# Kernel tuning notes

Hardware: AMD Instinct MI355X
Metric: run time of the kernel (lower is better)

The kernel has to match this reference:

```python
import jax, jax.numpy as jnp
import numpy as np
from jax import lax

ROUTING_ITERS = 3
EPS = 1e-8


def _conv(x, w, b, stride=1):
    # x: [B,C,H,W], w: [O,C,kh,kw]  (VALID padding, NCHW/OIHW)
    y = lax.conv_general_dilated(x, w, (stride, stride), 'VALID',
                                 dimension_numbers=('NCHW', 'OIHW', 'NCHW'))
    return y + b[None, :, None, None]


def _maxpool2(x):
    return lax.reduce_window(x, -jnp.inf, lax.max, (1, 1, 2, 2), (1, 1, 2, 2), 'VALID')


def _squash(s, axis=-1):
    n2 = jnp.sum(s * s, axis=axis, keepdims=True)
    return s * (n2 / (1.0 + n2)) / jnp.sqrt(n2 + EPS)


def setup_inputs() -> dict:
    key = jax.random.key(0)
    ks = jax.random.split(key, 9)
    p = lambda k, shp: (jax.random.normal(k, shp, dtype=jnp.float32) * 0.05)
    return {
        'x':  jax.random.normal(ks[0], (64, 1, 92, 92), dtype=jnp.float32),
        'w1': p(ks[1], (128, 1, 9, 9)),   'b1': jnp.zeros((128,), jnp.float32),
        'w2': p(ks[2], (64, 128, 5, 5)),  'b2': jnp.zeros((64,), jnp.float32),
        'wc': p(ks[3], (128, 64, 8, 8)),  'bc': jnp.zeros((128,), jnp.float32),
        # routing transform: [num_primary=1024, num_sar=10, out_dim=16, in_dim=32]
        'Wr': p(ks[4], (1024, 10, 16, 32)),
    }


def reference(x, w1, b1, w2, b2, wc, bc, Wr):
    B = x.shape[0]
    # feature extractor (dropout is identity at inference)
    h = jax.nn.relu(_conv(x, w1, b1))          # [B,128,84,84]
    h = _maxpool2(h)                            # [B,128,42,42]
    h = _conv(h, w2, b2)                        # [B,64,38,38]
    # primary capsule conv
    h = _conv(h, wc, bc, stride=2)              # [B,128,16,16]
    # 128 channels = 4 capsule types * 32-dim capsules, 16x16 spatial -> 1024 caps
    u = h.reshape(B, 4, 32, 16, 16).transpose(0, 1, 3, 4, 2).reshape(B, 1024, 32)
    u = _squash(u)                              # [B,1024,32]
    # u_hat: predictions of each primary cap for each SAR cap
    u_hat = jnp.einsum('bpi,ptoi->bpto', u, Wr)  # [B,1024,10,16]
    # dynamic routing
    b_log = jnp.zeros((B, 1024, 10), dtype=x.dtype)
    for _ in range(ROUTING_ITERS):
        c = jax.nn.softmax(b_log, axis=2)               # [B,1024,10]
        s = jnp.einsum('bpt,bpto->bto', c, u_hat)       # [B,10,16]
        v = _squash(s)                                   # [B,10,16]
        b_log = b_log + jnp.einsum('bpto,bto->bpt', u_hat, v)
    likelihood = jnp.sqrt(jnp.sum(v * v, axis=-1) + EPS)  # [B,10]
    return likelihood
```

## Files before the change

### kernel.cpp

```cpp
#include <hip/hip_runtime.h>
#include <hip/hip_bf16.h>
#include <math.h>


#define EPSF 1e-8f

typedef __bf16 bf16x8 __attribute__((ext_vector_type(8)));
typedef __bf16 bf16x4 __attribute__((ext_vector_type(4)));
typedef float floatx4 __attribute__((ext_vector_type(4)));
typedef float floatx16 __attribute__((ext_vector_type(16)));

__global__ __launch_bounds__(256) void k_t_all(const float* __restrict__ Wr,
                                               const float* __restrict__ wc,
                                               const float* __restrict__ w2,
                                               const float* __restrict__ w1,
                                               __bf16* __restrict__ wrb,
                                               __bf16* __restrict__ wca,
                                               __bf16* __restrict__ w2a,
                                               __bf16* __restrict__ w1b) {
    int i = blockIdx.x * 256 + threadIdx.x;
    if (i < 5242880) {
        wrb[i] = (__bf16)Wr[i];
        return;
    }
    int i2 = i - 5242880;
    if (i2 < 524288) {
        int j = i2 & 7, lane = (i2 >> 3) & 63, f = i2 >> 9;
        int ct = f & 3, ks = (f >> 2) & 1, khw = (f >> 3) & 63, icc = f >> 9;
        int c32 = lane & 31, h = lane >> 5;
        int oc = ct * 32 + c32;
        int ic = icc * 32 + ks * 16 + h * 8 + j;
        wca[i2] = (__bf16)wc[(oc * 64 + ic) * 64 + khw];
        return;
    }
    int i3 = i2 - 524288;
    if (i3 < 204800) {
        int j = i3 & 7, lane = (i3 >> 3) & 63, f = i3 >> 9;
        int mt = f & 1, ks = (f >> 1) & 3, rem = f >> 3;
        int khw = rem % 25, icc = rem / 25;
        int c32 = lane & 31, h = lane >> 5;
        int oc = mt * 32 + c32;
        int ic = icc * 64 + ks * 16 + h * 8 + j;
        w2a[i3] = (__bf16)w2[(oc * 128 + ic) * 25 + khw];
        return;
    }
    int i4 = i3 - 204800;
    if (i4 < 12288) {
        int kt = i4 >> 10, oc = (i4 >> 3) & 127, j = i4 & 7;
        int k = kt * 8 + j;
        w1b[i4] = (__bf16)(k < 81 ? w1[oc * 81 + k] : 0.f);
    }
}

__global__ __launch_bounds__(256, 3) void k_conv1_mfma(const float* __restrict__ x,
                                                       const __bf16* __restrict__ w1b,
                                                       const float* __restrict__ b1,
                                                       __bf16* __restrict__ h1n) {
    __shared__ float xs[960];
    __shared__ __bf16 Bl[18432];
    int py = blockIdx.x, ocg = blockIdx.y, b = blockIdx.z;
    int t = threadIdx.x;
    int lane = t & 63, w = t >> 6;
    int cc = lane & 15, q = lane >> 4;

    const float* xb = x + (size_t)b * 8464 + 2 * py * 92;
    for (int j = t; j < 920; j += 256) xs[j] = xb[j];

    int ocA = ocg * 64 + w * 16 + cc;
    bf16x8 af[3];
#pragma unroll
    for (int ks = 0; ks < 3; ++ks)
        af[ks] = *(const bf16x8*)(w1b + ((ks * 4 + q) * 128 + ocA) * 8);

    __syncthreads();

    if (t < 192) {
        int row = t / 96, pos = t - (t / 96) * 96;
        int sbase = row * 92 + pos;
        bool pvalid = pos < 84;
#pragma unroll
        for (int kt = 0; kt < 12; ++kt) {
            bf16x8 pk;
#pragma unroll
            for (int j = 0; j < 8; ++j) {
                int k = kt * 8 + j;
                int kh = k / 9, kw = k - kh * 9;
                float v = (pvalid && k < 81) ? xs[sbase + kh * 92 + kw] : 0.f;
                pk[j] = (__bf16)v;
            }
            *(bf16x8*)(Bl + ((kt * 2 + row) * 96 + pos) * 8) = pk;
        }
    }
    __syncthreads();

    floatx4 acc[2][6];
    const char* Bb = (const char*)Bl + cc * 16 + q * 3072;
#pragma unroll
    for (int rr = 0; rr < 2; ++rr)
#pragma unroll
        for (int n6 = 0; n6 < 6; ++n6) {
            floatx4 a = (floatx4){0.f, 0.f, 0.f, 0.f};
#pragma unroll
            for (int ks = 0; ks < 3; ++ks) {
                bf16x8 bf = *(const bf16x8*)(Bb + ks * 12288 + rr * 1536 + n6 * 256);
                a = __builtin_amdgcn_mfma_f32_16x16x32_bf16(af[ks], bf, a, 0, 0, 0);
            }
            acc[rr][n6] = a;
        }

    int oc0 = ocg * 64 + w * 16 + q * 4;
    float4 bv = *(const float4*)(b1 + oc0);
    size_t obase = (((size_t)b * 42 + py) * 42) * 128 + oc0;
#pragma unroll
    for (int n6 = 0; n6 < 6; ++n6) {
        bf16x4 pk;
#pragma unroll
        for (int r = 0; r < 4; ++r) {
            float vert = fmaxf(acc[0][n6][r], acc[1][n6][r]);
            float hz = fmaxf(vert, __shfl_xor(vert, 1, 64));
            float pooled = fmaxf(hz + ((const float*)&bv)[r], 0.f);
            pk[r] = (__bf16)pooled;
        }
        if ((cc & 1) == 0) {
            int px = n6 * 8 + (cc >> 1);
            if (px < 42)
                *(bf16x4*)(h1n + obase + (size_t)px * 128) = pk;
        }
    }
}

__global__ __launch_bounds__(256) void k_conv2(const __bf16* __restrict__ h1n,
                                               const __bf16* __restrict__ w2a,
                                               float* __restrict__ p01) {
    __shared__ __bf16 ins[25704];
    int g = blockIdx.x, b = blockIdx.y, icc = blockIdx.z;
    int row0 = g * 5;
    int t = threadIdx.x;
    int lane = t & 63, w = t >> 6;
    int c32 = lane & 31, h = lane >> 5;
    int validp = (g < 7) ? 190 : 114;
    int ic0 = icc * 64;

    int baseN[2], posi[2];
#pragma unroll
    for (int nt = 0; nt < 2; ++nt) {
        int pi = (w * 2 + nt) * 32 + c32;
        int pc = pi < validp ? pi : validp - 1;
        int r = pc / 38, c = pc - r * 38;
        posi[nt] = pi;
        baseN[nt] = (r * 42 + c) * 136 + h * 16;
    }

#pragma unroll
    for (int half = 0; half < 2; ++half) {
        uint4 rb[6];
        int lo[6];
#pragma unroll
        for (int k = 0; k < 6; ++k) {
            int j = (half * 6 + k) * 256 + t;
            if (j > 3023) j -= 256;
            int lr = j / 336, rem = j - lr * 336;
            int ix = rem >> 3, sb = rem & 7;
            int rg = row0 + lr; if (rg > 41) rg = 41;
            rb[k] = *(const uint4*)(h1n + ((((size_t)b * 42 + rg) * 42 + ix) * 128 + ic0 + sb * 8));
            lo[k] = (lr * 42 + ix) * 136 + sb * 16;
        }
#pragma unroll
        for (int k = 0; k < 6; ++k)
            *(uint4*)((char*)ins + lo[k]) = rb[k];
    }

    floatx16 acc[2][2];
#pragma unroll
    for (int mt = 0; mt < 2; ++mt)
#pragma unroll
        for (int nt = 0; nt < 2; ++nt)
#pragma unroll
            for (int i = 0; i < 16; ++i) acc[mt][nt][i] = 0.f;

    const __bf16* wic = w2a + (size_t)icc * 25 * 4096 + (lane << 3);

    bf16x8 abuf[3][8];
#pragma unroll
    for (int ks = 0; ks < 4; ++ks) {
        abuf[0][ks * 2]     = *(const bf16x8*)(wic + 0 * 4096 + ks * 1024);
        abuf[0][ks * 2 + 1] = *(const bf16x8*)(wic + 0 * 4096 + ks * 1024 + 512);
        abuf[1][ks * 2]     = *(const bf16x8*)(wic + 1 * 4096 + ks * 1024);
        abuf[1][ks * 2 + 1] = *(const bf16x8*)(wic + 1 * 4096 + ks * 1024 + 512);
    }

    __syncthreads();
#pragma unroll
    for (int khw = 0; khw < 25; ++khw) {
        if (khw + 2 < 25) {
            const __bf16* wk2 = wic + (khw + 2) * 4096;
#pragma unroll
            for (int ks = 0; ks < 4; ++ks) {
                abuf[(khw + 2) % 3][ks * 2]     = *(const bf16x8*)(wk2 + ks * 1024);
                abuf[(khw + 2) % 3][ks * 2 + 1] = *(const bf16x8*)(wk2 + ks * 1024 + 512);
            }
        }
        int kh = khw / 5, kw = khw - kh * 5;
        int doff = (kh * 42 + kw) * 136;
#pragma unroll
        for (int ks = 0; ks < 4; ++ks) {
            bf16x8 a0 = abuf[khw % 3][ks * 2];
            bf16x8 a1 = abuf[khw % 3][ks * 2 + 1];
#pragma unroll
            for (int nt = 0; nt < 2; ++nt) {
                bf16x8 bfr = *(const bf16x8*)((char*)ins + baseN[nt] + doff + ks * 32);
                acc[0][nt] = __builtin_amdgcn_mfma_f32_32x32x16_bf16(a0, bfr, acc[0][nt], 0, 0, 0);
                acc[1][nt] = __builtin_amdgcn_mfma_f32_32x32x16_bf16(a1, bfr, acc[1][nt], 0, 0, 0);
            }
        }
    }
    float* pdst = p01 + (size_t)icc * 5914624;
#pragma unroll
    for (int nt = 0; nt < 2; ++nt) {
        int pi = posi[nt];
        if (pi < validp) {
            int r = pi / 38, c = pi - r * 38;
            int oh = row0 + r;
            size_t obase = (((size_t)b * 38 + oh) * 38 + c) * 64;
#pragma unroll
            for (int mt = 0; mt < 2; ++mt) {
#pragma unroll
                for (int g2 = 0; g2 < 4; ++g2) {
                    int oc0 = mt * 32 + g2 * 8 + h * 4;
                    floatx4 pv;
                    pv[0] = acc[mt][nt][g2 * 4 + 0];
                    pv[1] = acc[mt][nt][g2 * 4 + 1];
                    pv[2] = acc[mt][nt][g2 * 4 + 2];
                    pv[3] = acc[mt][nt][g2 * 4 + 3];
                    *(floatx4*)(pdst + obase + oc0) = pv;
                }
            }
        }
    }
}

__global__ __launch_bounds__(256) void k_reduce_h2(const float* __restrict__ p01,
                                                   const float* __restrict__ b2,
                                                   __bf16* __restrict__ h2n) {
    int i = blockIdx.x * 256 + threadIdx.x;
    if (i >= 1478656) return;
    size_t e = (size_t)i * 4;
    floatx4 a = *(const floatx4*)(p01 + e);
    floatx4 b = *(const floatx4*)(p01 + 5914624 + e);
    floatx4 bv = *(const floatx4*)(b2 + ((i * 4) & 63));
    bf16x4 pk;
    pk.x = (__bf16)(a[0] + b[0] + bv[0]);
    pk.y = (__bf16)(a[1] + b[1] + bv[1]);
    pk.z = (__bf16)(a[2] + b[2] + bv[2]);
    pk.w = (__bf16)(a[3] + b[3] + bv[3]);
    *(bf16x4*)(h2n + e) = pk;
}

__global__ __launch_bounds__(256, 4) void k_convcaps(const __bf16* __restrict__ h2n,
                                                     const __bf16* __restrict__ wca,
                                                     float* __restrict__ pc) {
    __shared__ __bf16 ins[13680];
    int g = blockIdx.x, b = blockIdx.y, icc = blockIdx.z;
    int t = threadIdx.x;
    int lane = t & 63, ct = t >> 6;
    int c32 = lane & 31, h = lane >> 5;
    int rloc = c32 >> 4, cx = c32 & 15;
    int ic0 = icc * 32;

    floatx16 acc;
#pragma unroll
    for (int i = 0; i < 16; ++i) acc[i] = 0.f;

    int Bbase = (76 * rloc + cx) * 72 + h * 16;
    {
        uint4 rb[6];
        int lo[6];
#pragma unroll
        for (int k = 0; k < 6; ++k) {
            int j = k * 256 + t;
            if (j > 1519) j -= 256;
            int r = j / 152, rem = j - r * 152;
            int c = rem >> 2, s = rem & 3;
            rb[k] = *(const uint4*)(h2n + ((((size_t)b * 38 + 4 * g + r) * 38 + c) * 64 + ic0 + s * 8));
            int X = (r * 2 + (c & 1)) * 19 + (c >> 1);
            lo[k] = X * 72 + s * 16;
        }
#pragma unroll
        for (int k = 0; k < 6; ++k)
            *(uint4*)((char*)ins + lo[k]) = rb[k];
    }
    __syncthreads();
    const __bf16* wic = wca + ((size_t)icc * 64 * 8 + ct) * 512 + (lane << 3);
#pragma unroll
    for (int khw = 0; khw < 64; ++khw) {
        int kh = khw >> 3, kw = khw & 7;
        int par = kw & 1, k2 = kw >> 1;
        int doff = ((kh * 2 + par) * 19 + k2) * 72;
        const __bf16* wk = wic + khw * 4096;
#pragma unroll
        for (int ks = 0; ks < 2; ++ks) {
            bf16x8 af = *(const bf16x8*)(wk + ks * 2048);
            bf16x8 bfr = *(const bf16x8*)((char*)ins + Bbase + doff + ks * 32);
            acc = __builtin_amdgcn_mfma_f32_32x32x16_bf16(af, bfr, acc, 0, 0, 0);
        }
    }
    int pos = (2 * g + rloc) * 16 + cx;
    float* dst = pc + (size_t)icc * 2097152 + (((size_t)b * 1024 + ct * 256 + pos) * 32);
#pragma unroll
    for (int g2 = 0; g2 < 4; ++g2) {
        floatx4 pv;
        pv[0] = acc[g2 * 4 + 0];
        pv[1] = acc[g2 * 4 + 1];
        pv[2] = acc[g2 * 4 + 2];
        pv[3] = acc[g2 * 4 + 3];
        *(floatx4*)(dst + g2 * 8 + h * 4) = pv;
    }
}

__global__ __launch_bounds__(256) void k_squash(const float* __restrict__ pc,
                                                const float* __restrict__ bc,
                                                __bf16* __restrict__ ub) {
    int i = blockIdx.x * 256 + threadIdx.x;
    if (i >= 65536) return;
    int ct = (i >> 8) & 3;
    const float* p0 = pc + (size_t)i * 32;
    const float* p1 = pc + 2097152 + (size_t)i * 32;
    const float* bv = bc + ct * 32;
    float vals[32];
    float n2 = 0.f;
#pragma unroll
    for (int k = 0; k < 8; ++k) {
        floatx4 a = *(const floatx4*)(p0 + k * 4);
        floatx4 b = *(const floatx4*)(p1 + k * 4);
        floatx4 bb = *(const floatx4*)(bv + k * 4);
#pragma unroll
        for (int e = 0; e < 4; ++e) {
            float v = a[e] + b[e] + bb[e];
            vals[k * 4 + e] = v;
            n2 = fmaf(v, v, n2);
        }
    }
    float scale = (n2 / (1.f + n2)) / sqrtf(n2 + EPSF);
    __bf16* dst = ub + (size_t)i * 32;
#pragma unroll
    for (int k = 0; k < 8; ++k) {
        bf16x4 pk;
        pk.x = (__bf16)(vals[k * 4 + 0] * scale);
        pk.y = (__bf16)(vals[k * 4 + 1] * scale);
        pk.z = (__bf16)(vals[k * 4 + 2] * scale);
        pk.w = (__bf16)(vals[k * 4 + 3] * scale);
        *(bf16x4*)(dst + k * 4) = pk;
    }
}

__global__ __launch_bounds__(256, 2) void k_uhat(const __bf16* __restrict__ ub,
                                                 const __bf16* __restrict__ wrb,
                                                 __bf16* __restrict__ uhT) {
    int pt = blockIdx.x, ts = blockIdx.y, bz = blockIdx.z;
    int t = threadIdx.x;
    int p = pt * 64 + (t & 63);
    int q = t >> 6;
    bf16x8 wf[4][4];
#pragma unroll
    for (int o4 = 0; o4 < 4; ++o4)
#pragma unroll
        for (int j = 0; j < 4; ++j)
            wf[o4][j] = *(const bf16x8*)(wrb + (((size_t)p * 10 + ts) * 16 + q * 4 + o4) * 32 + j * 8);
#pragma unroll 1
    for (int bi = 0; bi < 16; ++bi) {
        int b = bz * 16 + bi;
        bf16x8 uf[4];
        const bf16x8* up = (const bf16x8*)(ub + ((size_t)b * 1024 + p) * 32);
#pragma unroll
        for (int j = 0; j < 4; ++j) uf[j] = up[j];
#pragma unroll
        for (int o4 = 0; o4 < 4; ++o4) {
            float s = 0.f;
#pragma unroll
            for (int j = 0; j < 4; ++j)
#pragma unroll
                for (int e = 0; e < 8; ++e)
                    s = fmaf((float)uf[j][e], (float)wf[o4][j][e], s);
            uhT[(((size_t)b * 10 + ts) * 16 + q * 4 + o4) * 1024 + p] = (__bf16)s;
        }
    }
}

__global__ __launch_bounds__(256) void k_route(const __bf16* __restrict__ uhT,
                                               const float* __restrict__ blR,
                                               float* __restrict__ blW,
                                               float* __restrict__ out,
                                               int first, int dob, int last) {
    __shared__ __bf16 uh_s[16384];
    __shared__ float sred[4][16];
    __shared__ float vs[16];
    int b = blockIdx.x, tt = blockIdx.y;
    int t = threadIdx.x;
    const __bf16* uhb = uhT + ((size_t)b * 10 + tt) * 16384;
#pragma unroll
    for (int k = 0; k < 8; ++k) {
        int j = k * 256 + t;
        *(uint4*)((char*)uh_s + j * 16) = *(const uint4*)((const char*)uhb + j * 16);
    }
    __syncthreads();

    float acc[16];
#pragma unroll
    for (int o = 0; o < 16; ++o) acc[o] = 0.f;
    const float* blb = blR + b * 10240;
    for (int p = t; p < 1024; p += 256) {
        float c;
        if (first) {
            c = 0.1f;
        } else {
            float den = 0.f, et = 0.f;
#pragma unroll
            for (int tp = 0; tp < 10; ++tp) {
                float e = expf(blb[tp * 1024 + p]);
                den += e;
                if (tp == tt) et = e;
            }
            c = et / den;
        }
#pragma unroll
        for (int o = 0; o < 16; ++o)
            acc[o] = fmaf(c, (float)uh_s[o * 1024 + p], acc[o]);
    }
    int lane = t & 63, wid = t >> 6;
#pragma unroll
    for (int o = 0; o < 16; ++o) {
        float v = acc[o];
#pragma unroll
        for (int off = 32; off >= 1; off >>= 1) v += __shfl_xor(v, off, 64);
        if (lane == 0) sred[wid][o] = v;
    }
    __syncthreads();
    if (t < 16) {
        float s = (sred[0][t] + sred[1][t]) + (sred[2][t] + sred[3][t]);
        float n2 = s * s;
#pragma unroll
        for (int off = 1; off < 16; off <<= 1) n2 += __shfl_xor(n2, off, 16);
        float scale = (n2 / (1.f + n2)) / sqrtf(n2 + EPSF);
        vs[t] = s * scale;
        if (last && t == 0) {
            float sv2 = n2 * scale * scale;
            out[b * 10 + tt] = sqrtf(sv2 + EPSF);
        }
    }
    __syncthreads();

    if (dob) {
        const float* blr = blR + (b * 10 + tt) * 1024;
        float* blw = blW + (b * 10 + tt) * 1024;
        for (int p = t; p < 1024; p += 256) {
            float d = 0.f;
#pragma unroll
            for (int o = 0; o < 16; ++o) d = fmaf((float)uh_s[o * 1024 + p], vs[o], d);
            blw[p] = first ? d : (blr[p] + d);
        }
    }
}

extern "C" void kernel_launch(void* const* d_in, const int* in_sizes, int n_in,
                              void* d_out, int out_size, void* d_ws, size_t ws_size,
                              hipStream_t stream) {
    const float* x  = (const float*)d_in[0];
    const float* w1 = (const float*)d_in[1];
    const float* b1 = (const float*)d_in[2];
    const float* w2 = (const float*)d_in[3];
    const float* b2 = (const float*)d_in[4];
    const float* wc = (const float*)d_in[5];
    const float* bc = (const float*)d_in[6];
    const float* Wr = (const float*)d_in[7];
    float* out = (float*)d_out;
    float* ws  = (float*)d_ws;

    __bf16* w2a = (__bf16*)(ws);
    __bf16* wca = (__bf16*)(ws + 102400);
    __bf16* w1b = (__bf16*)(ws + 364544);
    __bf16* h1n = (__bf16*)(ws + 375040);
    __bf16* h2n = (__bf16*)(ws + 7600384);
    __bf16* ub  = (__bf16*)(ws + 12654848);
    float*  blA = ws + 14752000;
    __bf16* wrb = (__bf16*)(ws + 15417600);
    float*  p01 = ws + 18039040;
    float*  pc  = ws + 18039040;
    float*  blB = ws + 29868288;
    __bf16* uhT = (__bf16*)(ws + 375040);

    k_t_all<<<23376, 256, 0, stream>>>(Wr, wc, w2, w1, wrb, wca, w2a, w1b);
    k_conv1_mfma<<<dim3(42, 2, 64), 256, 0, stream>>>(x, w1b, b1, h1n);
    k_conv2<<<dim3(8, 64, 2), 256, 0, stream>>>(h1n, w2a, p01);
    k_reduce_h2<<<5776, 256, 0, stream>>>(p01, b2, h2n);
    k_convcaps<<<dim3(8, 64, 2), 256, 0, stream>>>(h2n, wca, pc);
    k_squash<<<256, 256, 0, stream>>>(pc, bc, ub);
    k_uhat<<<dim3(16, 10, 4), 256, 0, stream>>>(ub, wrb, uhT);
    k_route<<<dim3(64, 10), 256, 0, stream>>>(uhT, blA, blA, out, 1, 1, 0);
    k_route<<<dim3(64, 10), 256, 0, stream>>>(uhT, blA, blB, out, 0, 1, 0);
    k_route<<<dim3(64, 10), 256, 0, stream>>>(uhT, blB, blB, out, 0, 0, 1);
}
```

Measured before the change: 289.2 us.

## Trim conv2 to three waves and ping-pong prefetch weights in conv kernels

```diff
diff --git a/kernel.cpp b/kernel.cpp
--- a/kernel.cpp
+++ b/kernel.cpp
@@ -129,9 +129,9 @@
     }
 }
 
-__global__ __launch_bounds__(256) void k_conv2(const __bf16* __restrict__ h1n,
-                                               const __bf16* __restrict__ w2a,
-                                               float* __restrict__ p01) {
+__global__ __launch_bounds__(192, 2) void k_conv2(const __bf16* __restrict__ h1n,
+                                                  const __bf16* __restrict__ w2a,
+                                                  float* __restrict__ p01) {
     __shared__ __bf16 ins[25704];
     int g = blockIdx.x, b = blockIdx.y, icc = blockIdx.z;
     int row0 = g * 5;
@@ -153,12 +153,12 @@
 
 #pragma unroll
     for (int half = 0; half < 2; ++half) {
-        uint4 rb[6];
-        int lo[6];
-#pragma unroll
-        for (int k = 0; k < 6; ++k) {
-            int j = (half * 6 + k) * 256 + t;
-            if (j > 3023) j -= 256;
+        uint4 rb[8];
+        int lo[8];
+#pragma unroll
+        for (int k = 0; k < 8; ++k) {
+            int j = (half * 8 + k) * 192 + t;
+            if (j > 3023) j -= 192;
             int lr = j / 336, rem = j - lr * 336;
             int ix = rem >> 3, sb = rem & 7;
             int rg = row0 + lr; if (rg > 41) rg = 41;
@@ -166,7 +166,7 @@
             lo[k] = (lr * 42 + ix) * 136 + sb * 16;
         }
 #pragma unroll
-        for (int k = 0; k < 6; ++k)
+        for (int k = 0; k < 8; ++k)
             *(uint4*)((char*)ins + lo[k]) = rb[k];
     }
 
@@ -180,40 +180,54 @@
 
     const __bf16* wic = w2a + (size_t)icc * 25 * 4096 + (lane << 3);
 
-    bf16x8 abuf[3][8];
+    bf16x8 pa[8], pb[8];
 #pragma unroll
     for (int ks = 0; ks < 4; ++ks) {
-        abuf[0][ks * 2]     = *(const bf16x8*)(wic + 0 * 4096 + ks * 1024);
-        abuf[0][ks * 2 + 1] = *(const bf16x8*)(wic + 0 * 4096 + ks * 1024 + 512);
-        abuf[1][ks * 2]     = *(const bf16x8*)(wic + 1 * 4096 + ks * 1024);
-        abuf[1][ks * 2 + 1] = *(const bf16x8*)(wic + 1 * 4096 + ks * 1024 + 512);
-    }
-
-    __syncthreads();
-#pragma unroll
-    for (int khw = 0; khw < 25; ++khw) {
-        if (khw + 2 < 25) {
-            const __bf16* wk2 = wic + (khw + 2) * 4096;
-#pragma unroll
-            for (int ks = 0; ks < 4; ++ks) {
-                abuf[(khw + 2) % 3][ks * 2]     = *(const bf16x8*)(wk2 + ks * 1024);
-                abuf[(khw + 2) % 3][ks * 2 + 1] = *(const bf16x8*)(wk2 + ks * 1024 + 512);
-            }
-        }
-        int kh = khw / 5, kw = khw - kh * 5;
-        int doff = (kh * 42 + kw) * 136;
-#pragma unroll
-        for (int ks = 0; ks < 4; ++ks) {
-            bf16x8 a0 = abuf[khw % 3][ks * 2];
-            bf16x8 a1 = abuf[khw % 3][ks * 2 + 1];
-#pragma unroll
-            for (int nt = 0; nt < 2; ++nt) {
-                bf16x8 bfr = *(const bf16x8*)((char*)ins + baseN[nt] + doff + ks * 32);
-                acc[0][nt] = __builtin_amdgcn_mfma_f32_32x32x16_bf16(a0, bfr, acc[0][nt], 0, 0, 0);
-                acc[1][nt] = __builtin_amdgcn_mfma_f32_32x32x16_bf16(a1, bfr, acc[1][nt], 0, 0, 0);
-            }
-        }
-    }
+        pa[ks * 2]     = *(const bf16x8*)(wic + ks * 1024);
+        pa[ks * 2 + 1] = *(const bf16x8*)(wic + ks * 1024 + 512);
+    }
+
+    __syncthreads();
+
+#define CONV2_MFMA(BUF, KHW)                                                   \
+    {                                                                          \
+        int kh = (KHW) / 5, kw = (KHW) - kh * 5;                               \
+        int doff = (kh * 42 + kw) * 136;                                       \
+        _Pragma("unroll")                                                      \
+        for (int ks = 0; ks < 4; ++ks) {                                       \
+            bf16x8 a0 = BUF[ks * 2];                                           \
+            bf16x8 a1 = BUF[ks * 2 + 1];                                       \
+            _Pragma("unroll")                                                  \
+            for (int nt = 0; nt < 2; ++nt) {                                   \
+                bf16x8 bfr = *(const bf16x8*)((char*)ins + baseN[nt] + doff + ks * 32); \
+                acc[0][nt] = __builtin_amdgcn_mfma_f32_32x32x16_bf16(a0, bfr, acc[0][nt], 0, 0, 0); \
+                acc[1][nt] = __builtin_amdgcn_mfma_f32_32x32x16_bf16(a1, bfr, acc[1][nt], 0, 0, 0); \
+            }                                                                  \
+        }                                                                      \
+    }
+
+#define CONV2_LOAD(BUF, KHW)                                                   \
+    {                                                                          \
+        const __bf16* wk_ = wic + (KHW) * 4096;                                \
+        _Pragma("unroll")                                                      \
+        for (int ks = 0; ks < 4; ++ks) {                                       \
+            BUF[ks * 2]     = *(const bf16x8*)(wk_ + ks * 1024);               \
+            BUF[ks * 2 + 1] = *(const bf16x8*)(wk_ + ks * 1024 + 512);         \
+        }                                                                      \
+    }
+
+#pragma unroll
+    for (int kk = 0; kk < 24; kk += 2) {
+        CONV2_LOAD(pb, kk + 1);
+        CONV2_MFMA(pa, kk);
+        int nx = (kk + 2 < 25) ? kk + 2 : 24;
+        CONV2_LOAD(pa, nx);
+        CONV2_MFMA(pb, kk + 1);
+    }
+    CONV2_MFMA(pa, 24);
+#undef CONV2_MFMA
+#undef CONV2_LOAD
+
     float* pdst = p01 + (size_t)icc * 5914624;
 #pragma unroll
     for (int nt = 0; nt < 2; ++nt) {
@@ -289,21 +303,45 @@
         for (int k = 0; k < 6; ++k)
             *(uint4*)((char*)ins + lo[k]) = rb[k];
     }
-    __syncthreads();
+
     const __bf16* wic = wca + ((size_t)icc * 64 * 8 + ct) * 512 + (lane << 3);
-#pragma unroll
-    for (int khw = 0; khw < 64; ++khw) {
-        int kh = khw >> 3, kw = khw & 7;
-        int par = kw & 1, k2 = kw >> 1;
-        int doff = ((kh * 2 + par) * 19 + k2) * 72;
-        const __bf16* wk = wic + khw * 4096;
-#pragma unroll
-        for (int ks = 0; ks < 2; ++ks) {
-            bf16x8 af = *(const bf16x8*)(wk + ks * 2048);
-            bf16x8 bfr = *(const bf16x8*)((char*)ins + Bbase + doff + ks * 32);
-            acc = __builtin_amdgcn_mfma_f32_32x32x16_bf16(af, bfr, acc, 0, 0, 0);
-        }
-    }
+    bf16x8 qa[2], qb[2];
+    qa[0] = *(const bf16x8*)(wic);
+    qa[1] = *(const bf16x8*)(wic + 2048);
+    __syncthreads();
+
+#define CC_MFMA(BUF, KHW)                                                      \
+    {                                                                          \
+        int kh = (KHW) >> 3, kw = (KHW) & 7;                                   \
+        int par = kw & 1, k2 = kw >> 1;                                        \
+        int doff = ((kh * 2 + par) * 19 + k2) * 72;                            \
+        _Pragma("unroll")                                                      \
+        for (int ks = 0; ks < 2; ++ks) {                                       \
+            bf16x8 bfr = *(const bf16x8*)((char*)ins + Bbase + doff + ks * 32); \
+            acc = __builtin_amdgcn_mfma_f32_32x32x16_bf16(BUF[ks], bfr, acc, 0, 0, 0); \
+        }                                                                      \
+    }
+
+#define CC_LOAD(BUF, KHW)                                                      \
+    {                                                                          \
+        const __bf16* wk_ = wic + (KHW) * 4096;                                \
+        BUF[0] = *(const bf16x8*)(wk_);                                        \
+        BUF[1] = *(const bf16x8*)(wk_ + 2048);                                 \
+    }
+
+#pragma unroll
+    for (int kk = 0; kk < 62; kk += 2) {
+        CC_LOAD(qb, kk + 1);
+        CC_MFMA(qa, kk);
+        CC_LOAD(qa, kk + 2);
+        CC_MFMA(qb, kk + 1);
+    }
+    CC_LOAD(qb, 63);
+    CC_MFMA(qa, 62);
+    CC_MFMA(qb, 63);
+#undef CC_MFMA
+#undef CC_LOAD
+
     int pos = (2 * g + rloc) * 16 + cx;
     float* dst = pc + (size_t)icc * 2097152 + (((size_t)b * 1024 + ct * 256 + pos) * 32);
 #pragma unroll
@@ -490,7 +528,7 @@
 
     k_t_all<<<23376, 256, 0, stream>>>(Wr, wc, w2, w1, wrb, wca, w2a, w1b);
     k_conv1_mfma<<<dim3(42, 2, 64), 256, 0, stream>>>(x, w1b, b1, h1n);
-    k_conv2<<<dim3(8, 64, 2), 256, 0, stream>>>(h1n, w2a, p01);
+    k_conv2<<<dim3(8, 64, 2), 192, 0, stream>>>(h1n, w2a, p01);
     k_reduce_h2<<<5776, 256, 0, stream>>>(p01, b2, h2n);
     k_convcaps<<<dim3(8, 64, 2), 256, 0, stream>>>(h2n, wca, pc);
     k_squash<<<256, 256, 0, stream>>>(pc, bc, ub);
```

Result: slower. 296.9 us (+2.7%).
